# Kernel optimization log

Measured on AMD Instinct MI355X. Metric: run time of the kernel, lower is better.

Reference implementation:

```python
import jax, jax.numpy as jnp
import numpy as np

EMBD_D = 384
HEAD_SIZE = 64  # 384 // 6


def setup_inputs() -> dict:
    key = jax.random.key(0)
    kx, kq, kk, kv = jax.random.split(key, 4)
    B, T = 16, 2048
    x = jax.random.normal(kx, (B, T, EMBD_D), dtype=jnp.float32)
    s = 1.0 / np.sqrt(EMBD_D)
    Wq = jax.random.normal(kq, (EMBD_D, HEAD_SIZE), dtype=jnp.float32) * s
    Wk = jax.random.normal(kk, (EMBD_D, HEAD_SIZE), dtype=jnp.float32) * s
    Wv = jax.random.normal(kv, (EMBD_D, HEAD_SIZE), dtype=jnp.float32) * s
    return {"x": x, "Wq": Wq, "Wk": Wk, "Wv": Wv}


def reference(x, Wq, Wk, Wv):
    # x: [B,T,C]; projections to head_size=64 (Linear, no bias)
    q = jnp.einsum("btc,cd->btd", x, Wq)
    k = jnp.einsum("btc,cd->btd", x, Wk)
    v = jnp.einsum("btc,cd->btd", x, Wv)
    scale = jnp.asarray(HEAD_SIZE, q.dtype) ** -0.5
    qk = jnp.einsum("btd,bsd->bts", q, k) * scale  # [B,T,T]
    # Faithful to original quirk: tril then mask exact zeros to -inf
    masked = jnp.tril(qk)
    masked = jnp.where(masked == 0, -jnp.inf, masked)
    scores = jax.nn.softmax(masked, axis=-1)
    # dropout is identity in eval mode (reference baseline)
    return jnp.einsum("bts,bsd->btd", scores, v)
```

## Files before the change

kernel.cpp:

```cpp
#include <hip/hip_runtime.h>

typedef short bf16x8 __attribute__((ext_vector_type(8)));
typedef float f32x4 __attribute__((ext_vector_type(4)));
typedef unsigned int u32;
typedef __attribute__((address_space(1))) const u32 gu32;
typedef __attribute__((address_space(3))) u32 lu32;

#define NEG_INF (-__builtin_inff())

static __device__ __forceinline__ unsigned short f2bf(float f) {
  union { float f; unsigned u; } v; v.f = f;
  return (unsigned short)((v.u + 0x7fffu + ((v.u >> 16) & 1u)) >> 16);
}
static __device__ __forceinline__ unsigned fbits(float f) {
  union { float f; unsigned u; } v; v.f = f;
  return v.u;
}
static __device__ __forceinline__ unsigned pack2(float a, float b) {
  return __builtin_amdgcn_perm(fbits(b) + 0x8000u, fbits(a) + 0x8000u, 0x07060302u);
}
static __device__ __forceinline__ f32x4 mfma16(bf16x8 a, bf16x8 b, f32x4 c) {
  return __builtin_amdgcn_mfma_f32_16x16x32_bf16(a, b, c, 0, 0, 0);
}
static __device__ __forceinline__ void dma16(const void* g, void* l) {
  __builtin_amdgcn_global_load_lds((gu32*)g, (lu32*)l, 16, 0, 0);
}

__global__ __launch_bounds__(256) void prep_w(const float* __restrict__ wq,
                                              const float* __restrict__ wk,
                                              const float* __restrict__ wv,
                                              char* __restrict__ wt) {
  int i = blockIdx.x * 256 + threadIdx.x;
  if (i >= 384 * 64) return;
  int c = i >> 6, d = i & 63;
  int c6 = c >> 6, cin = c & 63;
  const float Cs = 0.18033688011112042f;
  long base = (long)(c6 * 192) * 128;
  int col = (cin * 2) ^ ((d & 7) << 4);
  *(unsigned short*)(wt + base + (long)d * 128 + col) = f2bf(wq[i] * Cs);
  *(unsigned short*)(wt + base + (long)(64 + d) * 128 + col) = f2bf(wk[i]);
  *(unsigned short*)(wt + base + (long)(128 + d) * 128 + col) = f2bf(wv[i]);
}

__global__ __launch_bounds__(256, 2) void proj_kernel(
    const float* __restrict__ x, const char* __restrict__ wt,
    unsigned short* __restrict__ qo, char* __restrict__ kT,
    char* __restrict__ vT) {
  __shared__ char wls[2][24576];
  const int tid = threadIdx.x;
  const int wave = tid >> 6, lane = tid & 63;
  const int lo = lane & 15, quad = lane >> 4;
  const long tok0 = ((long)blockIdx.x * 4 + wave) * 16;

#pragma unroll
  for (int s2 = 0; s2 < 6; ++s2) {
    const int s = wave * 6 + s2;
    dma16(wt + s * 1024 + lane * 16, &wls[0][s * 1024]);
  }
  bf16x8 ax[12];
  const float* xr = x + (tok0 + lo) * 384 + quad * 8;
#pragma unroll
  for (int kk = 0; kk < 12; ++kk) {
    float4 x0 = *(const float4*)(xr + kk * 32);
    float4 x1 = *(const float4*)(xr + kk * 32 + 4);
    bf16x8 a;
    a[0] = (short)f2bf(x0.x); a[1] = (short)f2bf(x0.y);
    a[2] = (short)f2bf(x0.z); a[3] = (short)f2bf(x0.w);
    a[4] = (short)f2bf(x1.x); a[5] = (short)f2bf(x1.y);
    a[6] = (short)f2bf(x1.z); a[7] = (short)f2bf(x1.w);
    ax[kk] = a;
  }

  f32x4 acc[12];
#pragma unroll
  for (int nt = 0; nt < 12; ++nt) acc[nt] = (f32x4){0.f, 0.f, 0.f, 0.f};

  for (int c6 = 0; c6 < 6; ++c6) {
    const int buf = c6 & 1;
    __syncthreads();
    if (c6 < 5) {
      const char* wg = wt + (long)(c6 + 1) * 24576;
#pragma unroll
      for (int s2 = 0; s2 < 6; ++s2) {
        const int s = wave * 6 + s2;
        dma16(wg + s * 1024 + lane * 16, &wls[buf ^ 1][s * 1024]);
      }
    }
#pragma unroll
    for (int kk = 0; kk < 2; ++kk) {
      const bf16x8 axk = ax[c6 * 2 + kk];
#pragma unroll
      for (int nt = 0; nt < 12; ++nt) {
        const int dd = nt * 16 + lo;
        const int col = ((kk * 4 + quad) ^ (lo & 7)) << 4;
        bf16x8 wf = *(const bf16x8*)(&wls[buf][dd * 128 + col]);
        if (nt < 8)
          acc[nt] = mfma16(wf, axk, acc[nt]);
        else
          acc[nt] = mfma16(axk, wf, acc[nt]);
      }
    }
  }

  const long bb = tok0 >> 11;
  const int tin0 = (int)(tok0 & 2047);
  const int kt = tin0 >> 6;
  const long tile = ((bb * 32 + kt) << 13);
  const int key0w = (tin0 & 63) + quad * 4;
  const int keyl = (tin0 & 63) + lo;
#pragma unroll
  for (int nt = 0; nt < 12; ++nt) {
    uint2 uu;
    uu.x = pack2(acc[nt][0], acc[nt][1]);
    uu.y = pack2(acc[nt][2], acc[nt][3]);
    if (nt < 4) {
      *(uint2*)(qo + (tok0 + lo) * 64 + nt * 16 + quad * 4) = uu;
    } else if (nt < 8) {
      const int d0 = (nt - 4) * 16 + quad * 4;
      *(uint2*)(kT + tile + keyl * 128 + (((d0 * 2) ^ ((keyl & 7) << 4)))) = uu;
    } else {
      const int d = (nt - 8) * 16 + lo;
      *(uint2*)(vT + tile + d * 128 + (((key0w * 2) ^ ((d & 7) << 4)))) = uu;
    }
  }
}

__global__ __launch_bounds__(256, 2) void attn_kernel(
    const unsigned short* __restrict__ qg, const char* __restrict__ kT,
    const char* __restrict__ vT, float* __restrict__ out) {
  __shared__ char kls[2][2][8192];
  __shared__ char vls[2][2][8192];
  __shared__ unsigned short ps[4][16][72];

  const int tid = threadIdx.x;
  const int h = tid >> 6, lane = tid & 63;
  const int lo = lane & 15, quad = lane >> 4;
  const int b = blockIdx.x & 15;
  const int idx = blockIdx.x >> 4;
  const int a = (blockIdx.x < 256) ? (31 - idx) : (idx - 16);
  const int j = 4 * a + h;
  const int niter = a + 1;
  const int nstage = (niter + 1) >> 1;
  const int qrow0 = j * 16;

  const unsigned short* qb = qg + (long)b * 2048 * 64;
  const char* kbT = kT + ((long)b * 32 << 13);
  const char* vbT = vT + ((long)b * 32 << 13);
  float* ob = out + (long)b * 2048 * 64;

  const unsigned short* qr = qb + (long)(qrow0 + lo) * 64 + quad * 8;
  const bf16x8 bq0 = *(const bf16x8*)qr;
  const bf16x8 bq1 = *(const bf16x8*)(qr + 32);

#pragma unroll
  for (int tt = 0; tt < 2; ++tt) {
    const char* kg = kbT + ((long)tt << 13);
    const char* vg = vbT + ((long)tt << 13);
#pragma unroll
    for (int s2 = 0; s2 < 2; ++s2) {
      const int s = h * 2 + s2;
      dma16(kg + s * 1024 + lane * 16, &kls[0][tt][s * 1024]);
      dma16(vg + s * 1024 + lane * 16, &vls[0][tt][s * 1024]);
    }
  }

  f32x4 oacc[4];
#pragma unroll
  for (int dt = 0; dt < 4; ++dt) oacc[dt] = (f32x4){0.f, 0.f, 0.f, 0.f};
  float l = 0.f;
  const int swz = (lo & 7);
  const int qrl = qrow0 + lo;

  for (int st = 0; st < nstage; ++st) {
    const int buf = st & 1;
    __syncthreads();
    if (st + 1 < nstage) {
#pragma unroll
      for (int tt = 0; tt < 2; ++tt) {
        const int tn = 2 * st + 2 + tt;
        const char* kg = kbT + ((long)tn << 13);
        const char* vg = vbT + ((long)tn << 13);
#pragma unroll
        for (int s2 = 0; s2 < 2; ++s2) {
          const int s = h * 2 + s2;
          dma16(kg + s * 1024 + lane * 16, &kls[buf ^ 1][tt][s * 1024]);
          dma16(vg + s * 1024 + lane * 16, &vls[buf ^ 1][tt][s * 1024]);
        }
      }
    }
#pragma unroll
    for (int tt = 0; tt < 2; ++tt) {
      const int kt = 2 * st + tt;
      if (kt >= niter) break;
      const bool diag = (kt == niter - 1);
      const int key0 = kt * 64;

#pragma unroll
      for (int t = 0; t < 4; ++t) {
        const int row = (t * 16 + lo) * 128;
        bf16x8 ak0 = *(const bf16x8*)(&kls[buf][tt][row + ((quad ^ swz) << 4)]);
        bf16x8 ak1 = *(const bf16x8*)(&kls[buf][tt][row + (((4 + quad) ^ swz) << 4)]);
        f32x4 s = (f32x4){0.f, 0.f, 0.f, 0.f};
        s = mfma16(ak0, bq0, s);
        s = mfma16(ak1, bq1, s);
        if (diag) {
#pragma unroll
          for (int r = 0; r < 4; ++r)
            if (key0 + t * 16 + quad * 4 + r > qrl) s[r] = NEG_INF;
        }
        float e0 = __builtin_amdgcn_exp2f(s[0]);
        float e1 = __builtin_amdgcn_exp2f(s[1]);
        float e2 = __builtin_amdgcn_exp2f(s[2]);
        float e3 = __builtin_amdgcn_exp2f(s[3]);
        l += (e0 + e1) + (e2 + e3);
        uint2 uu;
        uu.x = pack2(e0, e1);
        uu.y = pack2(e2, e3);
        *(uint2*)&ps[h][lo][t * 16 + quad * 4] = uu;
      }
      asm volatile("s_waitcnt lgkmcnt(0)" ::: "memory");
#pragma unroll
      for (int kk2 = 0; kk2 < 2; ++kk2) {
        bf16x8 bp = *(const bf16x8*)&ps[h][lo][kk2 * 32 + quad * 8];
#pragma unroll
        for (int dt = 0; dt < 4; ++dt) {
          const int rowv = (dt * 16 + lo) * 128;
          bf16x8 av =
              *(const bf16x8*)(&vls[buf][tt][rowv + (((kk2 * 4 + quad) ^ swz) << 4)]);
          oacc[dt] = mfma16(av, bp, oacc[dt]);
        }
      }
    }
  }

  l += __shfl_xor(l, 16, 64);
  l += __shfl_xor(l, 32, 64);
  const float inv = 1.0f / l;
  float* orow = ob + (long)(qrow0 + lo) * 64;
#pragma unroll
  for (int dt = 0; dt < 4; ++dt) {
    float4 st;
    st.x = oacc[dt][0] * inv; st.y = oacc[dt][1] * inv;
    st.z = oacc[dt][2] * inv; st.w = oacc[dt][3] * inv;
    *(float4*)(orow + dt * 16 + quad * 4) = st;
  }
}

extern "C" void kernel_launch(void* const* d_in, const int* in_sizes, int n_in,
                              void* d_out, int out_size, void* d_ws, size_t ws_size,
                              hipStream_t stream) {
  const float* x = (const float*)d_in[0];
  const float* wq = (const float*)d_in[1];
  const float* wk = (const float*)d_in[2];
  const float* wv = (const float*)d_in[3];
  float* out = (float*)d_out;

  char* ws = (char*)d_ws;
  char* wt = ws;
  const size_t MB4 = (size_t)4 * 1024 * 1024;
  unsigned short* qws = (unsigned short*)(ws + 147456);
  char* kT = ws + 147456 + MB4;
  char* vT = ws + 147456 + 2 * MB4;

  prep_w<<<96, 256, 0, stream>>>(wq, wk, wv, wt);
  proj_kernel<<<512, 256, 0, stream>>>(x, wt, qws, kT, vT);
  attn_kernel<<<512, 256, 0, stream>>>(qws, kT, vT, out);
}
```

Before: 127.3 us.

## Fuse weight prep, projection and attention into one cooperative kernel with grid syncs

Replaces the three separate launches (weight prep, QKV projection, attention) with a single cooperative kernel that runs each phase and separates them with grid-wide barriers. The x tile is loaded and converted to bf16 before the first barrier, so that load overlaps the weight prep. The aim is to remove inter-kernel launch gaps and tail effects. In exchange it relies on all 512 blocks being co-resident (two blocks per CU via launch bounds) and pays for two grid syncs. If the cooperative launch fails it falls back to the three-kernel path.

```diff
diff --git a/kernel.cpp b/kernel.cpp
--- a/kernel.cpp
+++ b/kernel.cpp
@@ -1,4 +1,7 @@
 #include <hip/hip_runtime.h>
+#include <hip/hip_cooperative_groups.h>
+
+namespace cg = cooperative_groups;
 
 typedef short bf16x8 __attribute__((ext_vector_type(8)));
 typedef float f32x4 __attribute__((ext_vector_type(4)));
@@ -24,6 +27,238 @@
 }
 static __device__ __forceinline__ void dma16(const void* g, void* l) {
   __builtin_amdgcn_global_load_lds((gu32*)g, (lu32*)l, 16, 0, 0);
+}
+
+__global__ __launch_bounds__(256, 2) void fused_kernel(
+    const float* __restrict__ x, const float* __restrict__ wq,
+    const float* __restrict__ wk, const float* __restrict__ wv,
+    char* __restrict__ wt, unsigned short* __restrict__ qo,
+    char* __restrict__ kT, char* __restrict__ vT, float* __restrict__ out) {
+  __shared__ __align__(16) union {
+    char wls[2][24576];
+    struct {
+      char kls[2][2][8192];
+      char vls[2][2][8192];
+      unsigned short ps[4][16][72];
+    } at;
+  } sm;
+
+  const int tid = threadIdx.x;
+  const int bid = blockIdx.x;
+  const int wave = tid >> 6, lane = tid & 63;
+  const int lo = lane & 15, quad = lane >> 4;
+
+  {
+    const int i = bid * 256 + tid;
+    if (i < 384 * 64) {
+      const int c = i >> 6, d = i & 63;
+      const int c6 = c >> 6, cin = c & 63;
+      const float Cs = 0.18033688011112042f;
+      const long base = (long)(c6 * 192) * 128;
+      const int col = (cin * 2) ^ ((d & 7) << 4);
+      *(unsigned short*)(wt + base + (long)d * 128 + col) = f2bf(wq[i] * Cs);
+      *(unsigned short*)(wt + base + (long)(64 + d) * 128 + col) = f2bf(wk[i]);
+      *(unsigned short*)(wt + base + (long)(128 + d) * 128 + col) = f2bf(wv[i]);
+    }
+  }
+
+  const long tok0 = ((long)bid * 4 + wave) * 16;
+  bf16x8 ax[12];
+  {
+    const float* xr = x + (tok0 + lo) * 384 + quad * 8;
+#pragma unroll
+    for (int kk = 0; kk < 12; ++kk) {
+      float4 x0 = *(const float4*)(xr + kk * 32);
+      float4 x1 = *(const float4*)(xr + kk * 32 + 4);
+      bf16x8 a2;
+      a2[0] = (short)f2bf(x0.x); a2[1] = (short)f2bf(x0.y);
+      a2[2] = (short)f2bf(x0.z); a2[3] = (short)f2bf(x0.w);
+      a2[4] = (short)f2bf(x1.x); a2[5] = (short)f2bf(x1.y);
+      a2[6] = (short)f2bf(x1.z); a2[7] = (short)f2bf(x1.w);
+      ax[kk] = a2;
+    }
+  }
+
+  __threadfence();
+  cg::this_grid().sync();
+  __threadfence();
+
+  {
+#pragma unroll
+    for (int s2 = 0; s2 < 6; ++s2) {
+      const int s = wave * 6 + s2;
+      dma16(wt + s * 1024 + lane * 16, &sm.wls[0][s * 1024]);
+    }
+    f32x4 acc[12];
+#pragma unroll
+    for (int nt = 0; nt < 12; ++nt) acc[nt] = (f32x4){0.f, 0.f, 0.f, 0.f};
+
+    for (int c6 = 0; c6 < 6; ++c6) {
+      const int buf = c6 & 1;
+      __syncthreads();
+      if (c6 < 5) {
+        const char* wg = wt + (long)(c6 + 1) * 24576;
+#pragma unroll
+        for (int s2 = 0; s2 < 6; ++s2) {
+          const int s = wave * 6 + s2;
+          dma16(wg + s * 1024 + lane * 16, &sm.wls[buf ^ 1][s * 1024]);
+        }
+      }
+#pragma unroll
+      for (int kk = 0; kk < 2; ++kk) {
+        const bf16x8 axk = ax[c6 * 2 + kk];
+#pragma unroll
+        for (int nt = 0; nt < 12; ++nt) {
+          const int dd = nt * 16 + lo;
+          const int col = ((kk * 4 + quad) ^ (lo & 7)) << 4;
+          bf16x8 wf = *(const bf16x8*)(&sm.wls[buf][dd * 128 + col]);
+          if (nt < 8)
+            acc[nt] = mfma16(wf, axk, acc[nt]);
+          else
+            acc[nt] = mfma16(axk, wf, acc[nt]);
+        }
+      }
+    }
+
+    const long bb = tok0 >> 11;
+    const int tin0 = (int)(tok0 & 2047);
+    const int ktile = tin0 >> 6;
+    const long tile = ((bb * 32 + ktile) << 13);
+    const int key0w = (tin0 & 63) + quad * 4;
+    const int keyl = (tin0 & 63) + lo;
+#pragma unroll
+    for (int nt = 0; nt < 12; ++nt) {
+      uint2 uu;
+      uu.x = pack2(acc[nt][0], acc[nt][1]);
+      uu.y = pack2(acc[nt][2], acc[nt][3]);
+      if (nt < 4) {
+        *(uint2*)(qo + (tok0 + lo) * 64 + nt * 16 + quad * 4) = uu;
+      } else if (nt < 8) {
+        const int d0 = (nt - 4) * 16 + quad * 4;
+        *(uint2*)(kT + tile + keyl * 128 + (((d0 * 2) ^ ((keyl & 7) << 4)))) = uu;
+      } else {
+        const int d = (nt - 8) * 16 + lo;
+        *(uint2*)(vT + tile + d * 128 + (((key0w * 2) ^ ((d & 7) << 4)))) = uu;
+      }
+    }
+  }
+
+  __threadfence();
+  cg::this_grid().sync();
+  __threadfence();
+
+  {
+    const int h = wave;
+    const int b = bid & 15;
+    const int idx = bid >> 4;
+    const int a = (bid < 256) ? (31 - idx) : (idx - 16);
+    const int j = 4 * a + h;
+    const int niter = a + 1;
+    const int nstage = (niter + 1) >> 1;
+    const int qrow0 = j * 16;
+
+    const unsigned short* qb = qo + (long)b * 2048 * 64;
+    const char* kbT = kT + ((long)b * 32 << 13);
+    const char* vbT = vT + ((long)b * 32 << 13);
+    float* ob = out + (long)b * 2048 * 64;
+
+    const unsigned short* qr = qb + (long)(qrow0 + lo) * 64 + quad * 8;
+    const bf16x8 bq0 = *(const bf16x8*)qr;
+    const bf16x8 bq1 = *(const bf16x8*)(qr + 32);
+
+#pragma unroll
+    for (int tt = 0; tt < 2; ++tt) {
+      const char* kg = kbT + ((long)tt << 13);
+      const char* vg = vbT + ((long)tt << 13);
+#pragma unroll
+      for (int s2 = 0; s2 < 2; ++s2) {
+        const int s = h * 2 + s2;
+        dma16(kg + s * 1024 + lane * 16, &sm.at.kls[0][tt][s * 1024]);
+        dma16(vg + s * 1024 + lane * 16, &sm.at.vls[0][tt][s * 1024]);
+      }
+    }
+
+    f32x4 oacc[4];
+#pragma unroll
+    for (int dt = 0; dt < 4; ++dt) oacc[dt] = (f32x4){0.f, 0.f, 0.f, 0.f};
+    float l = 0.f;
+    const int swz = (lo & 7);
+    const int qrl = qrow0 + lo;
+
+    for (int st = 0; st < nstage; ++st) {
+      const int buf = st & 1;
+      __syncthreads();
+      if (st + 1 < nstage) {
+#pragma unroll
+        for (int tt = 0; tt < 2; ++tt) {
+          const int tn = 2 * st + 2 + tt;
+          const char* kg = kbT + ((long)tn << 13);
+          const char* vg = vbT + ((long)tn << 13);
+#pragma unroll
+          for (int s2 = 0; s2 < 2; ++s2) {
+            const int s = h * 2 + s2;
+            dma16(kg + s * 1024 + lane * 16, &sm.at.kls[buf ^ 1][tt][s * 1024]);
+            dma16(vg + s * 1024 + lane * 16, &sm.at.vls[buf ^ 1][tt][s * 1024]);
+          }
+        }
+      }
+#pragma unroll
+      for (int tt = 0; tt < 2; ++tt) {
+        const int kt = 2 * st + tt;
+        if (kt >= niter) break;
+        const bool diag = (kt == niter - 1);
+        const int key0 = kt * 64;
+
+#pragma unroll
+        for (int t = 0; t < 4; ++t) {
+          const int row = (t * 16 + lo) * 128;
+          bf16x8 ak0 = *(const bf16x8*)(&sm.at.kls[buf][tt][row + ((quad ^ swz) << 4)]);
+          bf16x8 ak1 = *(const bf16x8*)(&sm.at.kls[buf][tt][row + (((4 + quad) ^ swz) << 4)]);
+          f32x4 s = (f32x4){0.f, 0.f, 0.f, 0.f};
+          s = mfma16(ak0, bq0, s);
+          s = mfma16(ak1, bq1, s);
+          if (diag) {
+#pragma unroll
+            for (int r = 0; r < 4; ++r)
+              if (key0 + t * 16 + quad * 4 + r > qrl) s[r] = NEG_INF;
+          }
+          float e0 = __builtin_amdgcn_exp2f(s[0]);
+          float e1 = __builtin_amdgcn_exp2f(s[1]);
+          float e2 = __builtin_amdgcn_exp2f(s[2]);
+          float e3 = __builtin_amdgcn_exp2f(s[3]);
+          l += (e0 + e1) + (e2 + e3);
+          uint2 uu;
+          uu.x = pack2(e0, e1);
+          uu.y = pack2(e2, e3);
+          *(uint2*)&sm.at.ps[h][lo][t * 16 + quad * 4] = uu;
+        }
+        asm volatile("s_waitcnt lgkmcnt(0)" ::: "memory");
+#pragma unroll
+        for (int kk2 = 0; kk2 < 2; ++kk2) {
+          bf16x8 bp = *(const bf16x8*)&sm.at.ps[h][lo][kk2 * 32 + quad * 8];
+#pragma unroll
+          for (int dt = 0; dt < 4; ++dt) {
+            const int rowv = (dt * 16 + lo) * 128;
+            bf16x8 av =
+                *(const bf16x8*)(&sm.at.vls[buf][tt][rowv + (((kk2 * 4 + quad) ^ swz) << 4)]);
+            oacc[dt] = mfma16(av, bp, oacc[dt]);
+          }
+        }
+      }
+    }
+
+    l += __shfl_xor(l, 16, 64);
+    l += __shfl_xor(l, 32, 64);
+    const float inv = 1.0f / l;
+    float* orow = ob + (long)(qrow0 + lo) * 64;
+#pragma unroll
+    for (int dt = 0; dt < 4; ++dt) {
+      float4 stv;
+      stv.x = oacc[dt][0] * inv; stv.y = oacc[dt][1] * inv;
+      stv.z = oacc[dt][2] * inv; stv.w = oacc[dt][3] * inv;
+      *(float4*)(orow + dt * 16 + quad * 4) = stv;
+    }
+  }
 }
 
 __global__ __launch_bounds__(256) void prep_w(const float* __restrict__ wq,
@@ -262,7 +497,14 @@
   char* kT = ws + 147456 + MB4;
   char* vT = ws + 147456 + 2 * MB4;
 
-  prep_w<<<96, 256, 0, stream>>>(wq, wk, wv, wt);
-  proj_kernel<<<512, 256, 0, stream>>>(x, wt, qws, kT, vT);
-  attn_kernel<<<512, 256, 0, stream>>>(qws, kT, vT, out);
-}
+  void* args[] = {(void*)&x,   (void*)&wq, (void*)&wk, (void*)&wv, (void*)&wt,
+                  (void*)&qws, (void*)&kT, (void*)&vT, (void*)&out};
+  hipError_t e = hipLaunchCooperativeKernel(
+      reinterpret_cast<const void*>(&fused_kernel), dim3(512), dim3(256), args,
+      0u, stream);
+  if (e != hipSuccess) {
+    prep_w<<<96, 256, 0, stream>>>(wq, wk, wv, wt);
+    proj_kernel<<<512, 256, 0, stream>>>(x, wt, qws, kT, vT);
+    attn_kernel<<<512, 256, 0, stream>>>(qws, kT, vT, out);
+  }
+}
```

Result: slower. 426.5 us (+235.1%).

## Load K/V fragments directly from global memory, dropping LDS double buffering

Applied to the files above, without the earlier changes.

Removes the shared-memory double-buffered K/V staging with async DMA and block-wide barriers. Each wave now reads its K and V MFMA fragments for each key tile straight from global memory into registers. This drops the __syncthreads and LDS traffic, but the four waves of a block re-read the same K/V from global/L2 and there is no prefetch overlap across iterations, so load latency is exposed.

```diff
diff --git a/kernel.cpp b/kernel.cpp
--- a/kernel.cpp
+++ b/kernel.cpp
@@ -128,8 +128,6 @@
 __global__ __launch_bounds__(256, 2) void attn_kernel(
     const unsigned short* __restrict__ qg, const char* __restrict__ kT,
     const char* __restrict__ vT, float* __restrict__ out) {
-  __shared__ char kls[2][2][8192];
-  __shared__ char vls[2][2][8192];
   __shared__ unsigned short ps[4][16][72];
 
   const int tid = threadIdx.x;
@@ -140,7 +138,6 @@
   const int a = (blockIdx.x < 256) ? (31 - idx) : (idx - 16);
   const int j = 4 * a + h;
   const int niter = a + 1;
-  const int nstage = (niter + 1) >> 1;
   const int qrow0 = j * 16;
 
   const unsigned short* qb = qg + (long)b * 2048 * 64;
@@ -152,18 +149,6 @@
   const bf16x8 bq0 = *(const bf16x8*)qr;
   const bf16x8 bq1 = *(const bf16x8*)(qr + 32);
 
-#pragma unroll
-  for (int tt = 0; tt < 2; ++tt) {
-    const char* kg = kbT + ((long)tt << 13);
-    const char* vg = vbT + ((long)tt << 13);
-#pragma unroll
-    for (int s2 = 0; s2 < 2; ++s2) {
-      const int s = h * 2 + s2;
-      dma16(kg + s * 1024 + lane * 16, &kls[0][tt][s * 1024]);
-      dma16(vg + s * 1024 + lane * 16, &vls[0][tt][s * 1024]);
-    }
-  }
-
   f32x4 oacc[4];
 #pragma unroll
   for (int dt = 0; dt < 4; ++dt) oacc[dt] = (f32x4){0.f, 0.f, 0.f, 0.f};
@@ -171,64 +156,57 @@
   const int swz = (lo & 7);
   const int qrl = qrow0 + lo;
 
-  for (int st = 0; st < nstage; ++st) {
-    const int buf = st & 1;
-    __syncthreads();
-    if (st + 1 < nstage) {
-#pragma unroll
-      for (int tt = 0; tt < 2; ++tt) {
-        const int tn = 2 * st + 2 + tt;
-        const char* kg = kbT + ((long)tn << 13);
-        const char* vg = vbT + ((long)tn << 13);
-#pragma unroll
-        for (int s2 = 0; s2 < 2; ++s2) {
-          const int s = h * 2 + s2;
-          dma16(kg + s * 1024 + lane * 16, &kls[buf ^ 1][tt][s * 1024]);
-          dma16(vg + s * 1024 + lane * 16, &vls[buf ^ 1][tt][s * 1024]);
-        }
-      }
-    }
-#pragma unroll
-    for (int tt = 0; tt < 2; ++tt) {
-      const int kt = 2 * st + tt;
-      if (kt >= niter) break;
-      const bool diag = (kt == niter - 1);
-      const int key0 = kt * 64;
-
-#pragma unroll
-      for (int t = 0; t < 4; ++t) {
-        const int row = (t * 16 + lo) * 128;
-        bf16x8 ak0 = *(const bf16x8*)(&kls[buf][tt][row + ((quad ^ swz) << 4)]);
-        bf16x8 ak1 = *(const bf16x8*)(&kls[buf][tt][row + (((4 + quad) ^ swz) << 4)]);
-        f32x4 s = (f32x4){0.f, 0.f, 0.f, 0.f};
-        s = mfma16(ak0, bq0, s);
-        s = mfma16(ak1, bq1, s);
-        if (diag) {
-#pragma unroll
-          for (int r = 0; r < 4; ++r)
-            if (key0 + t * 16 + quad * 4 + r > qrl) s[r] = NEG_INF;
-        }
-        float e0 = __builtin_amdgcn_exp2f(s[0]);
-        float e1 = __builtin_amdgcn_exp2f(s[1]);
-        float e2 = __builtin_amdgcn_exp2f(s[2]);
-        float e3 = __builtin_amdgcn_exp2f(s[3]);
-        l += (e0 + e1) + (e2 + e3);
-        uint2 uu;
-        uu.x = pack2(e0, e1);
-        uu.y = pack2(e2, e3);
-        *(uint2*)&ps[h][lo][t * 16 + quad * 4] = uu;
-      }
-      asm volatile("s_waitcnt lgkmcnt(0)" ::: "memory");
-#pragma unroll
-      for (int kk2 = 0; kk2 < 2; ++kk2) {
-        bf16x8 bp = *(const bf16x8*)&ps[h][lo][kk2 * 32 + quad * 8];
-#pragma unroll
-        for (int dt = 0; dt < 4; ++dt) {
-          const int rowv = (dt * 16 + lo) * 128;
-          bf16x8 av =
-              *(const bf16x8*)(&vls[buf][tt][rowv + (((kk2 * 4 + quad) ^ swz) << 4)]);
-          oacc[dt] = mfma16(av, bp, oacc[dt]);
-        }
+  for (int kt = 0; kt < niter; ++kt) {
+    const bool diag = (kt == niter - 1);
+    const int key0 = kt * 64;
+    const char* kg = kbT + ((long)kt << 13);
+    const char* vg = vbT + ((long)kt << 13);
+
+    bf16x8 akf[8];
+#pragma unroll
+    for (int t = 0; t < 4; ++t) {
+      const int row = (t * 16 + lo) * 128;
+      akf[2 * t] = *(const bf16x8*)(kg + row + ((quad ^ swz) << 4));
+      akf[2 * t + 1] = *(const bf16x8*)(kg + row + (((4 + quad) ^ swz) << 4));
+    }
+    bf16x8 avf[8];
+#pragma unroll
+    for (int kk2 = 0; kk2 < 2; ++kk2) {
+#pragma unroll
+      for (int dt = 0; dt < 4; ++dt) {
+        const int rowv = (dt * 16 + lo) * 128;
+        avf[kk2 * 4 + dt] =
+            *(const bf16x8*)(vg + rowv + (((kk2 * 4 + quad) ^ swz) << 4));
+      }
+    }
+
+#pragma unroll
+    for (int t = 0; t < 4; ++t) {
+      f32x4 s = (f32x4){0.f, 0.f, 0.f, 0.f};
+      s = mfma16(akf[2 * t], bq0, s);
+      s = mfma16(akf[2 * t + 1], bq1, s);
+      if (diag) {
+#pragma unroll
+        for (int r = 0; r < 4; ++r)
+          if (key0 + t * 16 + quad * 4 + r > qrl) s[r] = NEG_INF;
+      }
+      float e0 = __builtin_amdgcn_exp2f(s[0]);
+      float e1 = __builtin_amdgcn_exp2f(s[1]);
+      float e2 = __builtin_amdgcn_exp2f(s[2]);
+      float e3 = __builtin_amdgcn_exp2f(s[3]);
+      l += (e0 + e1) + (e2 + e3);
+      uint2 uu;
+      uu.x = pack2(e0, e1);
+      uu.y = pack2(e2, e3);
+      *(uint2*)&ps[h][lo][t * 16 + quad * 4] = uu;
+    }
+    asm volatile("s_waitcnt lgkmcnt(0)" ::: "memory");
+#pragma unroll
+    for (int kk2 = 0; kk2 < 2; ++kk2) {
+      bf16x8 bp = *(const bf16x8*)&ps[h][lo][kk2 * 32 + quad * 8];
+#pragma unroll
+      for (int dt = 0; dt < 4; ++dt) {
+        oacc[dt] = mfma16(avf[kk2 * 4 + dt], bp, oacc[dt]);
       }
     }
   }
```

Measured after the change: 127.3 us. Within noise of the previous version (+0.0%).
